# Optimization experiments

Hardware: AMD Instinct MI355X
Metric: run time of the kernel (lower is better)

## Reference

```python
import jax, jax.numpy as jnp
import numpy as np

B, T, F, G, H, N, C = 32, 64, 32, 32, 256, 20000, 32
EPS = 1e-5


def setup_inputs() -> dict:
    key = jax.random.key(0)
    ks = jax.random.split(key, 24)
    s = 0.05
    d = {}
    d["data_feats"] = jax.random.normal(ks[0], (B, T, F), jnp.float32)
    d["gat_output"] = jax.random.normal(ks[1], (B, N, G), jnp.float32)
    d["row_ids"] = jax.random.randint(ks[2], (B, T), 0, 2 * N, jnp.int32)
    d["node_ids"] = jax.random.randint(ks[3], (N,), 0, 2 * N, jnp.int32)
    # shared LSTM (2 layers): layer0 input F+G, layer1 input H; b = b_ih + b_hh fused
    d["shared_Wih0"] = jax.random.normal(ks[4], (4 * H, F + G)) * s
    d["shared_Whh0"] = jax.random.normal(ks[5], (4 * H, H)) * s
    d["shared_b0"] = jax.random.normal(ks[6], (4 * H,)) * s
    d["shared_Wih1"] = jax.random.normal(ks[7], (4 * H, H)) * s
    d["shared_Whh1"] = jax.random.normal(ks[8], (4 * H, H)) * s
    d["shared_b1"] = jax.random.normal(ks[9], (4 * H,)) * s
    # act/time/timeR LSTMs stacked on leading axis 3, each 2 layers of [4H,H]
    d["heads_Wih"] = jax.random.normal(ks[10], (3, 2, 4 * H, H)) * s
    d["heads_Whh"] = jax.random.normal(ks[11], (3, 2, 4 * H, H)) * s
    d["heads_b"] = jax.random.normal(ks[12], (3, 2, 4 * H)) * s
    d["bn_gnn_g"] = jnp.ones((G,), jnp.float32)
    d["bn_gnn_b"] = jnp.zeros((G,), jnp.float32)
    d["bn_shared_g"] = jnp.ones((H,), jnp.float32)
    d["bn_shared_b"] = jnp.zeros((H,), jnp.float32)
    d["heads_bn_g"] = jnp.ones((3, H), jnp.float32)
    d["heads_bn_b"] = jnp.zeros((3, H), jnp.float32)
    d["fc_act_W"] = jax.random.normal(ks[13], (C, H)) * s
    d["fc_act_b"] = jnp.zeros((C,), jnp.float32)
    d["fc_time_W"] = jax.random.normal(ks[14], (1, H)) * s
    d["fc_time_b"] = jnp.zeros((1,), jnp.float32)
    d["fc_timeR_W"] = jax.random.normal(ks[15], (1, H)) * s
    d["fc_timeR_b"] = jnp.zeros((1,), jnp.float32)
    return d


def batchnorm(x, gamma, beta):
    # BatchNorm1d training-mode: stats over (batch, length) per channel; x: [B, L, C]
    mean = jnp.mean(x, axis=(0, 1))
    var = jnp.var(x, axis=(0, 1))
    return (x - mean) * (gamma / jnp.sqrt(var + EPS)) + beta


def lstm_layer(x, Wih, Whh, b):
    # x: [B, T, Din]; PyTorch gate order i, f, g, o
    xp = jnp.einsum("btf,gf->btg", x, Wih) + b  # [B, T, 4H]
    h = Whh.shape[1]
    init = (jnp.zeros((x.shape[0], h), x.dtype), jnp.zeros((x.shape[0], h), x.dtype))

    def step(carry, xt):
        hprev, cprev = carry
        gates = xt + hprev @ Whh.T
        i, f, g, o = jnp.split(gates, 4, axis=-1)
        c = jax.nn.sigmoid(f) * cprev + jax.nn.sigmoid(i) * jnp.tanh(g)
        hnew = jax.nn.sigmoid(o) * jnp.tanh(c)
        return (hnew, c), hnew

    _, hs = jax.lax.scan(step, init, jnp.swapaxes(xp, 0, 1))
    return jnp.swapaxes(hs, 0, 1)  # [B, T, H]


def reference(data_feats, gat_output, row_ids, node_ids,
              shared_Wih0, shared_Whh0, shared_b0,
              shared_Wih1, shared_Whh1, shared_b1,
              heads_Wih, heads_Whh, heads_b,
              bn_gnn_g, bn_gnn_b, bn_shared_g, bn_shared_b,
              heads_bn_g, heads_bn_b,
              fc_act_W, fc_act_b, fc_time_W, fc_time_b, fc_timeR_W, fc_timeR_b):
    # --- graph branch: BN over GAT output, value-match lookup + gather ---
    gat_norm = batchnorm(gat_output, bn_gnn_g, bn_gnn_b)  # [B, N, G]
    eq = row_ids[:, :, None] == node_ids[None, None, :]   # [B, T, N]
    idx = jnp.argmax(eq, axis=-1)                          # first matching index
    found = jnp.any(eq, axis=-1)
    gathered = jnp.take_along_axis(gat_norm, idx[:, :, None], axis=1)  # [B, T, G]
    matched = jnp.where(found[:, :, None], gathered, 0.0)
    lstm_in = jnp.concatenate([data_feats, matched], axis=-1)  # [B, T, F+G]

    # --- shared 2-layer LSTM + BN (dropout off / eval) ---
    shared = lstm_layer(lstm_in, shared_Wih0, shared_Whh0, shared_b0)
    shared = lstm_layer(shared, shared_Wih1, shared_Whh1, shared_b1)
    shared = batchnorm(shared, bn_shared_g, bn_shared_b)

    # --- act / time / timeR head LSTMs (vmapped over the 3 heads) + BN ---
    def head(Wih, Whh, b, g, bb):
        hh = lstm_layer(shared, Wih[0], Whh[0], b[0])
        hh = lstm_layer(hh, Wih[1], Whh[1], b[1])
        return batchnorm(hh, g, bb)

    heads = jax.vmap(head)(heads_Wih, heads_Whh, heads_b, heads_bn_g, heads_bn_b)
    last = heads[:, :, -1, :]  # [3, B, H]

    act = jax.nn.softmax(last[0] @ fc_act_W.T + fc_act_b, axis=1)
    time = last[1] @ fc_time_W.T + fc_time_b
    timeR = last[2] @ fc_timeR_W.T + fc_timeR_b
    return act, time, timeR
```

## Files before the change

### kernel.cpp

```cpp
#include <hip/hip_runtime.h>
#include <hip/hip_fp16.h>
#include <math.h>

#define Bn 32
#define Tn 64
#define Fdim 32
#define Gdim 32
#define Hdim 256
#define Ndim 20000
#define Cdim 32
#define G4 1024
#define BT 2048
#define EPSc 1e-5f

__device__ __forceinline__ float sigmoidf_(float x){ return 1.0f/(1.0f + __expf(-x)); }
__device__ __forceinline__ float tanhf_(float x){ return 2.0f/(1.0f+__expf(-2.0f*x)) - 1.0f; }

typedef _Float16 h2t __attribute__((ext_vector_type(2)));

__device__ __forceinline__ float fdot2_(unsigned w, unsigned h, float acc){
#if defined(__has_builtin) && __has_builtin(__builtin_amdgcn_fdot2)
  return __builtin_amdgcn_fdot2(__builtin_bit_cast(h2t, w), __builtin_bit_cast(h2t, h), acc, false);
#else
  h2t a = __builtin_bit_cast(h2t, w), b = __builtin_bit_cast(h2t, h);
  acc = fmaf((float)a.x, (float)b.x, acc);
  return fmaf((float)a.y, (float)b.y, acc);
#endif
}

__device__ __forceinline__ unsigned packh_(float lo, float hi){
  unsigned ulo = (unsigned)__half_as_ushort(__float2half(lo));
  unsigned uhi = (unsigned)__half_as_ushort(__float2half(hi));
  return ulo | (uhi << 16);
}

__global__ void init_kernel(float* ws){
  int i = blockIdx.x*256 + threadIdx.x;
  if (i < 2112) ws[i] = 0.0f;
  int* table = (int*)(ws + 2112);
  if (i < 40000) table[i] = 0x7fffffff;
}

__global__ void bn_stats_kernel(const float* __restrict__ gat, float* __restrict__ sums){
  __shared__ float ss[256], sq[256];
  int tid = threadIdx.x;
  int idx = blockIdx.x*256 + tid;
  int stride = gridDim.x*256;
  const int total = Bn*Ndim*Gdim;
  float s=0.f,q=0.f;
  for (int i=idx; i<total; i+=stride){ float v = gat[i]; s+=v; q+=v*v; }
  ss[tid]=s; sq[tid]=q; __syncthreads();
  for (int off=128; off>=32; off>>=1){
    if(tid<off){ ss[tid]+=ss[tid+off]; sq[tid]+=sq[tid+off]; }
    __syncthreads();
  }
  if (tid<32){ atomicAdd(&sums[tid], ss[tid]); atomicAdd(&sums[32+tid], sq[tid]); }
}

__global__ void table_kernel(const int* __restrict__ node_ids, int* __restrict__ table){
  int i = blockIdx.x*256 + threadIdx.x;
  if (i < Ndim) atomicMin(&table[node_ids[i]], i);
}

__global__ void build_input_kernel(const float* __restrict__ feats, const float* __restrict__ gat,
    const int* __restrict__ row_ids, const int* __restrict__ table, const float* __restrict__ sums,
    const float* __restrict__ bng, const float* __restrict__ bnb, unsigned* __restrict__ out){
  int gt = blockIdx.x*256 + threadIdx.x;
  int pos = gt >> 5; int k2 = gt & 31;
  float lo, hi;
  if (k2 < 16){
    float2 v = *(const float2*)(feats + pos*Fdim + 2*k2);
    lo = v.x; hi = v.y;
  } else {
    int g0 = 2*(k2-16);
    int r = row_ids[pos];
    int idx = table[r];
    if (idx < Ndim){
      int b = pos / Tn;
      float2 x = *(const float2*)(gat + (size_t)(b*Ndim + idx)*Gdim + g0);
      const float cnt = (float)(Bn*Ndim);
      float m0 = sums[g0]/cnt,   v0 = sums[32+g0]/cnt - m0*m0;
      float m1 = sums[g0+1]/cnt, v1 = sums[32+g0+1]/cnt - m1*m1;
      lo = (x.x-m0)*bng[g0]*rsqrtf(v0+EPSc) + bnb[g0];
      hi = (x.y-m1)*bng[g0+1]*rsqrtf(v1+EPSc) + bnb[g0+1];
    } else { lo = 0.0f; hi = 0.0f; }
  }
  out[gt] = packh_(lo, hi);
}

struct TArgs { const float* src[8]; unsigned* dst[8]; int K[8]; };
__global__ void packwih_kernel(TArgs a){
  __shared__ unsigned tile[32][33];
  int mat = blockIdx.y;
  int K = a.K[mat];
  int K2 = K >> 1;
  int ktiles = K2 >> 5;
  int tk = blockIdx.x & 3;
  int tn = blockIdx.x >> 2;
  if (tk >= ktiles) return;
  const float* src = a.src[mat];
  unsigned* dst = a.dst[mat];
  int tx = threadIdx.x, ty = threadIdx.y;
  int n0 = tn*32, k2_0 = tk*32;
  #pragma unroll
  for (int i=0;i<4;i++){
    int nn = ty + 8*i;
    const float* p = src + (size_t)(n0+nn)*K + 2*(k2_0 + tx);
    tile[nn][tx] = packh_(p[0], p[1]);
  }
  __syncthreads();
  #pragma unroll
  for (int i=0;i<4;i++){
    int r = ty + 8*i;
    dst[(size_t)(k2_0 + r)*G4 + n0 + tx] = tile[tx][r];
  }
}

struct PkArgs { const float* src[8]; };
__global__ void pack_kernel(PkArgs a, unsigned* __restrict__ dst){
  int gid = blockIdx.x*256 + threadIdx.x;
  int m = gid >> 17;
  int rem = gid & 0x1FFFF;
  int q = rem & 3;
  int t2 = (rem >> 2) & 1023;
  int ci = rem >> 12;
  int c = ci >> 3, i = ci & 7;
  int j = t2 & 255, kq = t2 >> 8;
  int r = 4*j + c;
  int k = kq*64 + 8*i + 2*q;
  const float* W = a.src[m];
  dst[gid] = packh_(W[r*256 + k], W[r*256 + k + 1]);
}

struct PArgs { const unsigned* x[3]; const unsigned* wt[3]; const float* bias[3]; float* out[3]; int K2; };
__global__ __launch_bounds__(256) void proj_kernel(PArgs a){
  int hd = blockIdx.z;
  int n  = blockIdx.y*256 + threadIdx.x;
  int m0 = blockIdx.x*8;
  int K2 = a.K2;
  const unsigned* xh = a.x[hd] + (size_t)m0*K2;
  const unsigned* wt = a.wt[hd];
  float bv = a.bias[hd][n];
  float acc[8];
  #pragma unroll
  for (int i=0;i<8;i++) acc[i]=bv;
  for (int k2=0;k2<K2;k2+=4){
    unsigned w0 = wt[(size_t)(k2+0)*G4+n];
    unsigned w1 = wt[(size_t)(k2+1)*G4+n];
    unsigned w2 = wt[(size_t)(k2+2)*G4+n];
    unsigned w3 = wt[(size_t)(k2+3)*G4+n];
    #pragma unroll
    for (int i=0;i<8;i++){
      uint4 xv = *(const uint4*)(xh + i*K2 + k2);
      acc[i]=fdot2_(w0,xv.x,acc[i]); acc[i]=fdot2_(w1,xv.y,acc[i]);
      acc[i]=fdot2_(w2,xv.z,acc[i]); acc[i]=fdot2_(w3,xv.w,acc[i]);
    }
  }
  float* out = a.out[hd] + (size_t)m0*G4 + n;
  #pragma unroll
  for (int i=0;i<8;i++) out[i*G4]=acc[i];
}

struct RArgs { const float* xp[3]; const unsigned* wt[3]; float* out[3]; unsigned* outh[3]; int f32out; int f16out; };
__global__ __launch_bounds__(1024,1) void rec_kernel(RArgs a){
  extern __shared__ float lds[];
  unsigned* lw   = (unsigned*)lds;
  float*    part = lds + 32768;
  unsigned* hp   = (unsigned*)(lds + 36864);
  int b = blockIdx.x, hd = blockIdx.y, tid = threadIdx.x;
  int j = tid & 255, kq = tid >> 8;
  const float* xp = a.xp[hd] + (size_t)b*Tn*G4;
  const unsigned* wt = a.wt[hd];
  float* out = a.out[hd] + (size_t)b*Tn*Hdim;
  unsigned* outh = a.outh[hd] + (size_t)b*Tn*128;
  int f32o = a.f32out, f16o = a.f16out;

  unsigned w[96];
  #pragma unroll
  for (int c=0;c<4;c++){
    #pragma unroll
    for (int i=0;i<6;i++){
      uint4 v = *(const uint4*)(wt + ((c*8+i)*1024 + tid)*4);
      w[(c*6+i)*4+0]=v.x; w[(c*6+i)*4+1]=v.y; w[(c*6+i)*4+2]=v.z; w[(c*6+i)*4+3]=v.w;
    }
    #pragma unroll
    for (int i=6;i<8;i++){
      uint4 v = *(const uint4*)(wt + ((c*8+i)*1024 + tid)*4);
      *(uint4*)(lw + ((c*2+(i-6))*1024 + tid)*4) = v;
    }
  }
  float cst = 0.0f;
  if (tid < 128){ hp[tid] = 0u; hp[128+tid] = 0u; }
  float4 xc = make_float4(0.f,0.f,0.f,0.f);
  if (kq == 0) xc = *(const float4*)(xp + 4*j);
  __syncthreads();

  int p = 0;
  for (int t=0; t<Tn; t++){
    float4 xn = xc;
    if (kq == 0) xn = *(const float4*)(xp + (size_t)(t+1)*G4 + 4*j);
    float ac0, ac1, ac2, ac3;
    if (kq == 0){ ac0=xc.x; ac1=xc.y; ac2=xc.z; ac3=xc.w; }
    else        { ac0=0.f; ac1=0.f; ac2=0.f; ac3=0.f; }
    const unsigned* hrow = hp + p*128 + kq*32;
    #pragma unroll
    for (int ic=0; ic<6; ic++){
      uint4 hv = *(const uint4*)(hrow + 4*ic);
      ac0=fdot2_(w[0*24+ic*4+0],hv.x,ac0); ac0=fdot2_(w[0*24+ic*4+1],hv.y,ac0);
      ac0=fdot2_(w[0*24+ic*4+2],hv.z,ac0); ac0=fdot2_(w[0*24+ic*4+3],hv.w,ac0);
      ac1=fdot2_(w[1*24+ic*4+0],hv.x,ac1); ac1=fdot2_(w[1*24+ic*4+1],hv.y,ac1);
      ac1=fdot2_(w[1*24+ic*4+2],hv.z,ac1); ac1=fdot2_(w[1*24+ic*4+3],hv.w,ac1);
      ac2=fdot2_(w[2*24+ic*4+0],hv.x,ac2); ac2=fdot2_(w[2*24+ic*4+1],hv.y,ac2);
      ac2=fdot2_(w[2*24+ic*4+2],hv.z,ac2); ac2=fdot2_(w[2*24+ic*4+3],hv.w,ac2);
      ac3=fdot2_(w[3*24+ic*4+0],hv.x,ac3); ac3=fdot2_(w[3*24+ic*4+1],hv.y,ac3);
      ac3=fdot2_(w[3*24+ic*4+2],hv.z,ac3); ac3=fdot2_(w[3*24+ic*4+3],hv.w,ac3);
    }
    #pragma unroll
    for (int ic=6; ic<8; ic++){
      uint4 hv = *(const uint4*)(hrow + 4*ic);
      { uint4 lv = *(const uint4*)(lw + ((0*2+(ic-6))*1024 + tid)*4);
        ac0=fdot2_(lv.x,hv.x,ac0); ac0=fdot2_(lv.y,hv.y,ac0);
        ac0=fdot2_(lv.z,hv.z,ac0); ac0=fdot2_(lv.w,hv.w,ac0); }
      { uint4 lv = *(const uint4*)(lw + ((1*2+(ic-6))*1024 + tid)*4);
        ac1=fdot2_(lv.x,hv.x,ac1); ac1=fdot2_(lv.y,hv.y,ac1);
        ac1=fdot2_(lv.z,hv.z,ac1); ac1=fdot2_(lv.w,hv.w,ac1); }
      { uint4 lv = *(const uint4*)(lw + ((2*2+(ic-6))*1024 + tid)*4);
        ac2=fdot2_(lv.x,hv.x,ac2); ac2=fdot2_(lv.y,hv.y,ac2);
        ac2=fdot2_(lv.z,hv.z,ac2); ac2=fdot2_(lv.w,hv.w,ac2); }
      { uint4 lv = *(const uint4*)(lw + ((3*2+(ic-6))*1024 + tid)*4);
        ac3=fdot2_(lv.x,hv.x,ac3); ac3=fdot2_(lv.y,hv.y,ac3);
        ac3=fdot2_(lv.z,hv.z,ac3); ac3=fdot2_(lv.w,hv.w,ac3); }
    }
    *(float4*)(part + kq*1024 + 4*j) = make_float4(ac0,ac1,ac2,ac3);
    asm volatile("s_waitcnt lgkmcnt(0)" ::: "memory");
    __builtin_amdgcn_s_barrier();
    if (tid < 256){
      int u = tid;
      float gi = part[u]     + part[1024+u]     + part[2048+u]     + part[3072+u];
      float gf = part[256+u] + part[1024+256+u] + part[2048+256+u] + part[3072+256+u];
      float gg = part[512+u] + part[1024+512+u] + part[2048+512+u] + part[3072+512+u];
      float go = part[768+u] + part[1024+768+u] + part[2048+768+u] + part[3072+768+u];
      cst = sigmoidf_(gf)*cst + sigmoidf_(gi)*tanhf_(gg);
      float h = sigmoidf_(go)*tanhf_(cst);
      if (f32o) out[t*Hdim + u] = h;
      float hpartner = __shfl_xor(h, 1);
      if ((u & 1) == 0){
        unsigned hh = packh_(h, hpartner);
        hp[(p^1)*128 + (u>>1)] = hh;
        if (f16o) outh[t*128 + (u>>1)] = hh;
      }
    }
    asm volatile("s_waitcnt lgkmcnt(0)" ::: "memory");
    __builtin_amdgcn_s_barrier();
    p ^= 1;
    xc = xn;
  }
}

struct SArgs { const float* in[3]; float* stats[3]; };
__global__ void stats_kernel(SArgs a){
  int hd = blockIdx.y; int tid = threadIdx.x;
  const float* in = a.in[hd] + blockIdx.x*256*Hdim;
  float s=0.f,q=0.f;
  for (int r=0;r<256;r++){ float v = in[r*Hdim + tid]; s+=v; q+=v*v; }
  atomicAdd(&a.stats[hd][tid], s);
  atomicAdd(&a.stats[hd][Hdim+tid], q);
}

__global__ void norm_kernel(const float* __restrict__ in, const float* __restrict__ stats,
   const float* __restrict__ g, const float* __restrict__ bta, unsigned* __restrict__ outh){
  int i2 = blockIdx.x*256 + threadIdx.x;
  int h2 = i2 & 127; int m = i2 >> 7;
  int h0 = 2*h2;
  float2 v = *(const float2*)(in + (size_t)m*Hdim + h0);
  float m0 = stats[h0]*(1.0f/BT),   v0 = stats[Hdim+h0]*(1.0f/BT) - m0*m0;
  float m1 = stats[h0+1]*(1.0f/BT), v1 = stats[Hdim+h0+1]*(1.0f/BT) - m1*m1;
  float lo = (v.x-m0)*g[h0]*rsqrtf(v0+EPSc) + bta[h0];
  float hi = (v.y-m1)*g[h0+1]*rsqrtf(v1+EPSc) + bta[h0+1];
  outh[i2] = packh_(lo, hi);
}

__global__ __launch_bounds__(256) void final_kernel(
  const float* __restrict__ h0, const float* __restrict__ h1, const float* __restrict__ h2,
  const float* __restrict__ stats,
  const float* __restrict__ hbg, const float* __restrict__ hbb,
  const float* __restrict__ actW, const float* __restrict__ actB,
  const float* __restrict__ tW, const float* __restrict__ tB,
  const float* __restrict__ rW, const float* __restrict__ rB,
  float* __restrict__ outp){
  __shared__ float v0[Bn*Hdim];
  __shared__ float lg[Bn*Cdim];
  int tid = threadIdx.x;
  for (int i=tid; i<Bn*Hdim; i+=256){
    int b=i>>8, h=i&255;
    float sm = stats[512 + h], sq = stats[512+256+h];
    float mean = sm*(1.0f/BT); float var = sq*(1.0f/BT) - mean*mean;
    v0[i] = (h0[(b*Tn+63)*Hdim + h] - mean)*hbg[h]*rsqrtf(var+EPSc) + hbb[h];
  }
  __syncthreads();
  for (int i=tid; i<Bn*Cdim; i+=256){
    int b=i>>5, cc=i&31;
    float acc = actB[cc];
    const float* wrow = actW + cc*Hdim;
    const float* vrow = v0 + b*Hdim;
    #pragma unroll 4
    for (int h=0;h<Hdim;h++) acc = fmaf(vrow[h], wrow[h], acc);
    lg[i] = acc;
  }
  __syncthreads();
  if (tid < Bn){
    int b = tid;
    float m = -1e30f;
    #pragma unroll
    for (int cc=0; cc<Cdim; cc++) m = fmaxf(m, lg[b*Cdim+cc]);
    float e[Cdim]; float s = 0.f;
    #pragma unroll
    for (int cc=0; cc<Cdim; cc++){ float ee = __expf(lg[b*Cdim+cc]-m); e[cc]=ee; s+=ee; }
    float inv = 1.0f/s;
    #pragma unroll
    for (int cc=0; cc<Cdim; cc++) outp[b*Cdim+cc] = e[cc]*inv;
  }
  if (tid < 64){
    int b = tid & 31; int w = tid >> 5;
    const float* hh = w ? h2 : h1;
    const float* fw = w ? rW : tW;
    float fb = w ? rB[0] : tB[0];
    int hd = 1 + w;
    float acc = fb;
    for (int h=0; h<Hdim; h++){
      float sm = stats[(1+hd)*512 + h], sq = stats[(1+hd)*512+256+h];
      float mean = sm*(1.0f/BT); float var = sq*(1.0f/BT) - mean*mean;
      float v = (hh[(b*Tn+63)*Hdim + h] - mean)*hbg[hd*Hdim+h]*rsqrtf(var+EPSc) + hbb[hd*Hdim+h];
      acc = fmaf(v, fw[h], acc);
    }
    outp[1024 + w*32 + b] = acc;
  }
}

extern "C" void kernel_launch(void* const* d_in, const int* in_sizes, int n_in,
                              void* d_out, int out_size, void* d_ws, size_t ws_size,
                              hipStream_t stream){
  const float* data_feats = (const float*)d_in[0];
  const float* gat   = (const float*)d_in[1];
  const int*   row_ids  = (const int*)d_in[2];
  const int*   node_ids = (const int*)d_in[3];
  const float* sWih0 = (const float*)d_in[4];
  const float* sWhh0 = (const float*)d_in[5];
  const float* sb0   = (const float*)d_in[6];
  const float* sWih1 = (const float*)d_in[7];
  const float* sWhh1 = (const float*)d_in[8];
  const float* sb1   = (const float*)d_in[9];
  const float* hWih  = (const float*)d_in[10];
  const float* hWhh  = (const float*)d_in[11];
  const float* hb    = (const float*)d_in[12];
  const float* bng   = (const float*)d_in[13];
  const float* bnb   = (const float*)d_in[14];
  const float* bsg   = (const float*)d_in[15];
  const float* bsb   = (const float*)d_in[16];
  const float* hbg   = (const float*)d_in[17];
  const float* hbb   = (const float*)d_in[18];
  const float* actW  = (const float*)d_in[19];
  const float* actB  = (const float*)d_in[20];
  const float* tW    = (const float*)d_in[21];
  const float* tB    = (const float*)d_in[22];
  const float* rW    = (const float*)d_in[23];
  const float* rB    = (const float*)d_in[24];
  float* ws  = (float*)d_ws;
  float* out = (float*)d_out;

  const size_t S_GAT = 0;
  const size_t S_BN  = 64;
  const size_t TABLE = 2112;
  const size_t WIHP  = 42112;
  const size_t PSLOT = 131072;
  const size_t WHHP  = WIHP + 8*PSLOT;
  const size_t LSTM_INH = WHHP + 8*PSLOT;
  const size_t XPOFF = LSTM_INH + 65536;
  const size_t BUF0H = XPOFF + 3*2097152;
  const size_t BUF1  = BUF0H + 262144;
  const size_t BUFNH = BUF1 + 524288;
  const size_t HB0H  = BUFNH + 262144;
  const size_t HB1   = HB0H + 3*262144;

  const int REC_LDS = 148480;
  hipFuncSetAttribute((const void*)rec_kernel, hipFuncAttributeMaxDynamicSharedMemorySize, REC_LDS);

  init_kernel<<<157,256,0,stream>>>(ws);
  bn_stats_kernel<<<2048,256,0,stream>>>(gat, ws+S_GAT);
  table_kernel<<<(Ndim+255)/256,256,0,stream>>>(node_ids, (int*)(ws+TABLE));
  build_input_kernel<<<256,256,0,stream>>>(data_feats, gat, row_ids, (int*)(ws+TABLE),
                                           ws+S_GAT, bng, bnb, (unsigned*)(ws+LSTM_INH));

  unsigned* wih = (unsigned*)(ws + WIHP);
  TArgs ta;
  ta.src[0]=sWih0; ta.K[0]=64;
  ta.src[1]=sWih1; ta.K[1]=256;
  for (int hd=0; hd<3; hd++) for (int l=0;l<2;l++){
    ta.src[2+hd*2+l] = hWih + (size_t)(hd*2+l)*G4*Hdim; ta.K[2+hd*2+l] = 256;
  }
  for (int i=0;i<8;i++) ta.dst[i] = wih + (size_t)i*PSLOT;
  packwih_kernel<<<dim3(128,8),dim3(32,8),0,stream>>>(ta);

  unsigned* whh = (unsigned*)(ws + WHHP);
  PkArgs pka;
  pka.src[0]=sWhh0; pka.src[1]=sWhh1;
  for (int hd=0; hd<3; hd++) for (int l=0;l<2;l++)
    pka.src[2+hd*2+l] = hWhh + (size_t)(hd*2+l)*G4*Hdim;
  pack_kernel<<<4096,256,0,stream>>>(pka, whh);

  PArgs pa; RArgs ra; SArgs sa;
  pa.K2=32; pa.x[0]=(unsigned*)(ws+LSTM_INH); pa.wt[0]=wih+0*PSLOT; pa.bias[0]=sb0; pa.out[0]=ws+XPOFF;
  proj_kernel<<<dim3(256,4,1),256,0,stream>>>(pa);
  ra.xp[0]=ws+XPOFF; ra.wt[0]=whh+0*PSLOT; ra.out[0]=ws+BUF1; ra.outh[0]=(unsigned*)(ws+BUF0H);
  ra.f32out=0; ra.f16out=1;
  rec_kernel<<<dim3(32,1),1024,REC_LDS,stream>>>(ra);
  pa.K2=128; pa.x[0]=(unsigned*)(ws+BUF0H); pa.wt[0]=wih+1*PSLOT; pa.bias[0]=sb1; pa.out[0]=ws+XPOFF;
  proj_kernel<<<dim3(256,4,1),256,0,stream>>>(pa);
  ra.xp[0]=ws+XPOFF; ra.wt[0]=whh+1*PSLOT; ra.out[0]=ws+BUF1; ra.outh[0]=(unsigned*)(ws+BUF0H);
  ra.f32out=1; ra.f16out=0;
  rec_kernel<<<dim3(32,1),1024,REC_LDS,stream>>>(ra);
  sa.in[0]=ws+BUF1; sa.stats[0]=ws+S_BN;
  stats_kernel<<<dim3(8,1),256,0,stream>>>(sa);
  norm_kernel<<<1024,256,0,stream>>>(ws+BUF1, ws+S_BN, bsg, bsb, (unsigned*)(ws+BUFNH));
  pa.K2=128;
  for (int hd=0;hd<3;hd++){
    pa.x[hd]=(unsigned*)(ws+BUFNH); pa.wt[hd]=wih+(size_t)(2+hd*2)*PSLOT; pa.bias[hd]=hb + (size_t)(hd*2)*G4;
    pa.out[hd]=ws+XPOFF+(size_t)hd*2097152;
  }
  proj_kernel<<<dim3(256,4,3),256,0,stream>>>(pa);
  for (int hd=0;hd<3;hd++){
    ra.xp[hd]=ws+XPOFF+(size_t)hd*2097152; ra.wt[hd]=whh+(size_t)(2+hd*2)*PSLOT;
    ra.out[hd]=ws+HB1+(size_t)hd*524288; ra.outh[hd]=(unsigned*)(ws+HB0H)+(size_t)hd*262144;
  }
  ra.f32out=0; ra.f16out=1;
  rec_kernel<<<dim3(32,3),1024,REC_LDS,stream>>>(ra);
  for (int hd=0;hd<3;hd++){
    pa.x[hd]=(unsigned*)(ws+HB0H)+(size_t)hd*262144; pa.wt[hd]=wih+(size_t)(2+hd*2+1)*PSLOT;
    pa.bias[hd]=hb + (size_t)(hd*2+1)*G4;
    pa.out[hd]=ws+XPOFF+(size_t)hd*2097152;
  }
  proj_kernel<<<dim3(256,4,3),256,0,stream>>>(pa);
  for (int hd=0;hd<3;hd++){
    ra.xp[hd]=ws+XPOFF+(size_t)hd*2097152; ra.wt[hd]=whh+(size_t)(2+hd*2+1)*PSLOT;
    ra.out[hd]=ws+HB1+(size_t)hd*524288; ra.outh[hd]=(unsigned*)(ws+HB0H)+(size_t)hd*262144;
  }
  ra.f32out=1; ra.f16out=0;
  rec_kernel<<<dim3(32,3),1024,REC_LDS,stream>>>(ra);
  for (int hd=0;hd<3;hd++){ sa.in[hd]=ws+HB1+(size_t)hd*524288; sa.stats[hd]=ws+S_BN+(size_t)(1+hd)*512; }
  stats_kernel<<<dim3(8,3),256,0,stream>>>(sa);
  final_kernel<<<1,256,0,stream>>>(ws+HB1, ws+HB1+524288, ws+HB1+2*524288, ws+S_BN,
                                   hbg, hbb, actW, actB, tW, tB, rW, rB, out);
}
```

Baseline: 898.7 us.

## Give each recurrent thread a full gate row and combine gates via DPP

The recurrent LSTM kernel is remapped so each of the 1024 threads computes one full gate row over all 256 hidden inputs, with the four gates of a unit sitting in adjacent lanes. The gate values are exchanged with DPP broadcasts instead of going through an LDS partial-sum buffer. This removes one barrier and the LDS reduction per timestep, and every thread now applies the nonlinearity. The weight packing kernel is rewritten to match the new layout. The cost is that every thread reads the whole hidden vector from LDS each step, and the next-step input prefetch is dropped.

```diff
diff --git a/kernel.cpp b/kernel.cpp
--- a/kernel.cpp
+++ b/kernel.cpp
@@ -32,6 +32,15 @@
   unsigned ulo = (unsigned)__half_as_ushort(__float2half(lo));
   unsigned uhi = (unsigned)__half_as_ushort(__float2half(hi));
   return ulo | (uhi << 16);
+}
+
+__device__ __forceinline__ float dppbc_(float y, int ctrl){
+  switch (ctrl){
+    case 0:  return __builtin_bit_cast(float, __builtin_amdgcn_mov_dpp(__builtin_bit_cast(int,y), 0x00, 0xF, 0xF, true));
+    case 1:  return __builtin_bit_cast(float, __builtin_amdgcn_mov_dpp(__builtin_bit_cast(int,y), 0x55, 0xF, 0xF, true));
+    case 2:  return __builtin_bit_cast(float, __builtin_amdgcn_mov_dpp(__builtin_bit_cast(int,y), 0xAA, 0xF, 0xF, true));
+    default: return __builtin_bit_cast(float, __builtin_amdgcn_mov_dpp(__builtin_bit_cast(int,y), 0xFF, 0xF, 0xF, true));
+  }
 }
 
 __global__ void init_kernel(float* ws){
@@ -120,16 +129,15 @@
 __global__ void pack_kernel(PkArgs a, unsigned* __restrict__ dst){
   int gid = blockIdx.x*256 + threadIdx.x;
   int m = gid >> 17;
-  int rem = gid & 0x1FFFF;
-  int q = rem & 3;
-  int t2 = (rem >> 2) & 1023;
-  int ci = rem >> 12;
-  int c = ci >> 3, i = ci & 7;
-  int j = t2 & 255, kq = t2 >> 8;
-  int r = 4*j + c;
-  int k = kq*64 + 8*i + 2*q;
+  int idx = gid & 0x1FFFF;
+  int e  = idx >> 12;
+  int t1 = (idx >> 2) & 1023;
+  int d4 = idx & 3;
+  int u = t1 >> 2, g = t1 & 3;
+  int rr = g*256 + u;
+  int k = 8*e + 2*d4;
   const float* W = a.src[m];
-  dst[gid] = packh_(W[r*256 + k], W[r*256 + k + 1]);
+  dst[gid] = packh_(W[rr*256 + k], W[rr*256 + k + 1]);
 }
 
 struct PArgs { const unsigned* x[3]; const unsigned* wt[3]; const float* bias[3]; float* out[3]; int K2; };
@@ -164,11 +172,11 @@
 struct RArgs { const float* xp[3]; const unsigned* wt[3]; float* out[3]; unsigned* outh[3]; int f32out; int f16out; };
 __global__ __launch_bounds__(1024,1) void rec_kernel(RArgs a){
   extern __shared__ float lds[];
-  unsigned* lw   = (unsigned*)lds;
-  float*    part = lds + 32768;
-  unsigned* hp   = (unsigned*)(lds + 36864);
+  unsigned* lw = (unsigned*)lds;
+  unsigned* hp = (unsigned*)lds + 32768;
   int b = blockIdx.x, hd = blockIdx.y, tid = threadIdx.x;
-  int j = tid & 255, kq = tid >> 8;
+  int u = tid >> 2, gsel = tid & 3;
+  int r = gsel*256 + u;
   const float* xp = a.xp[hd] + (size_t)b*Tn*G4;
   const unsigned* wt = a.wt[hd];
   float* out = a.out[hd] + (size_t)b*Tn*Hdim;
@@ -177,83 +185,63 @@
 
   unsigned w[96];
   #pragma unroll
-  for (int c=0;c<4;c++){
-    #pragma unroll
-    for (int i=0;i<6;i++){
-      uint4 v = *(const uint4*)(wt + ((c*8+i)*1024 + tid)*4);
-      w[(c*6+i)*4+0]=v.x; w[(c*6+i)*4+1]=v.y; w[(c*6+i)*4+2]=v.z; w[(c*6+i)*4+3]=v.w;
-    }
-    #pragma unroll
-    for (int i=6;i<8;i++){
-      uint4 v = *(const uint4*)(wt + ((c*8+i)*1024 + tid)*4);
-      *(uint4*)(lw + ((c*2+(i-6))*1024 + tid)*4) = v;
-    }
-  }
+  for (int e=0;e<24;e++){
+    uint4 v = *(const uint4*)(wt + (size_t)(e*1024 + tid)*4);
+    w[4*e+0]=v.x; w[4*e+1]=v.y; w[4*e+2]=v.z; w[4*e+3]=v.w;
+  }
+  #pragma unroll
+  for (int e=24;e<32;e++){
+    uint4 v = *(const uint4*)(wt + (size_t)(e*1024 + tid)*4);
+    *(uint4*)(lw + ((e-24)*1024 + tid)*4) = v;
+  }
+  if (tid < 256) hp[tid] = 0u;
   float cst = 0.0f;
-  if (tid < 128){ hp[tid] = 0u; hp[128+tid] = 0u; }
-  float4 xc = make_float4(0.f,0.f,0.f,0.f);
-  if (kq == 0) xc = *(const float4*)(xp + 4*j);
+  const float ab  = (gsel==2) ? 2.0f : 1.0f;
+  const float cof = (gsel==2) ? -1.0f : 0.0f;
   __syncthreads();
 
   int p = 0;
   for (int t=0; t<Tn; t++){
-    float4 xn = xc;
-    if (kq == 0) xn = *(const float4*)(xp + (size_t)(t+1)*G4 + 4*j);
-    float ac0, ac1, ac2, ac3;
-    if (kq == 0){ ac0=xc.x; ac1=xc.y; ac2=xc.z; ac3=xc.w; }
-    else        { ac0=0.f; ac1=0.f; ac2=0.f; ac3=0.f; }
-    const unsigned* hrow = hp + p*128 + kq*32;
-    #pragma unroll
-    for (int ic=0; ic<6; ic++){
-      uint4 hv = *(const uint4*)(hrow + 4*ic);
-      ac0=fdot2_(w[0*24+ic*4+0],hv.x,ac0); ac0=fdot2_(w[0*24+ic*4+1],hv.y,ac0);
-      ac0=fdot2_(w[0*24+ic*4+2],hv.z,ac0); ac0=fdot2_(w[0*24+ic*4+3],hv.w,ac0);
-      ac1=fdot2_(w[1*24+ic*4+0],hv.x,ac1); ac1=fdot2_(w[1*24+ic*4+1],hv.y,ac1);
-      ac1=fdot2_(w[1*24+ic*4+2],hv.z,ac1); ac1=fdot2_(w[1*24+ic*4+3],hv.w,ac1);
-      ac2=fdot2_(w[2*24+ic*4+0],hv.x,ac2); ac2=fdot2_(w[2*24+ic*4+1],hv.y,ac2);
-      ac2=fdot2_(w[2*24+ic*4+2],hv.z,ac2); ac2=fdot2_(w[2*24+ic*4+3],hv.w,ac2);
-      ac3=fdot2_(w[3*24+ic*4+0],hv.x,ac3); ac3=fdot2_(w[3*24+ic*4+1],hv.y,ac3);
-      ac3=fdot2_(w[3*24+ic*4+2],hv.z,ac3); ac3=fdot2_(w[3*24+ic*4+3],hv.w,ac3);
+    float xv = xp[(size_t)t*G4 + r];
+    const unsigned* hb = hp + p*128;
+    float acc0=0.f, acc1=0.f;
+    #pragma unroll
+    for (int j=0;j<24;j+=2){
+      uint4 h0 = *(const uint4*)(hb + 4*j);
+      uint4 h1 = *(const uint4*)(hb + 4*j + 4);
+      acc0=fdot2_(w[4*j+0],h0.x,acc0); acc1=fdot2_(w[4*j+4],h1.x,acc1);
+      acc0=fdot2_(w[4*j+1],h0.y,acc0); acc1=fdot2_(w[4*j+5],h1.y,acc1);
+      acc0=fdot2_(w[4*j+2],h0.z,acc0); acc1=fdot2_(w[4*j+6],h1.z,acc1);
+      acc0=fdot2_(w[4*j+3],h0.w,acc0); acc1=fdot2_(w[4*j+7],h1.w,acc1);
     }
     #pragma unroll
-    for (int ic=6; ic<8; ic++){
-      uint4 hv = *(const uint4*)(hrow + 4*ic);
-      { uint4 lv = *(const uint4*)(lw + ((0*2+(ic-6))*1024 + tid)*4);
-        ac0=fdot2_(lv.x,hv.x,ac0); ac0=fdot2_(lv.y,hv.y,ac0);
-        ac0=fdot2_(lv.z,hv.z,ac0); ac0=fdot2_(lv.w,hv.w,ac0); }
-      { uint4 lv = *(const uint4*)(lw + ((1*2+(ic-6))*1024 + tid)*4);
-        ac1=fdot2_(lv.x,hv.x,ac1); ac1=fdot2_(lv.y,hv.y,ac1);
-        ac1=fdot2_(lv.z,hv.z,ac1); ac1=fdot2_(lv.w,hv.w,ac1); }
-      { uint4 lv = *(const uint4*)(lw + ((2*2+(ic-6))*1024 + tid)*4);
-        ac2=fdot2_(lv.x,hv.x,ac2); ac2=fdot2_(lv.y,hv.y,ac2);
-        ac2=fdot2_(lv.z,hv.z,ac2); ac2=fdot2_(lv.w,hv.w,ac2); }
-      { uint4 lv = *(const uint4*)(lw + ((3*2+(ic-6))*1024 + tid)*4);
-        ac3=fdot2_(lv.x,hv.x,ac3); ac3=fdot2_(lv.y,hv.y,ac3);
-        ac3=fdot2_(lv.z,hv.z,ac3); ac3=fdot2_(lv.w,hv.w,ac3); }
+    for (int j=24;j<32;j+=2){
+      uint4 h0 = *(const uint4*)(hb + 4*j);
+      uint4 h1 = *(const uint4*)(hb + 4*j + 4);
+      uint4 l0 = *(const uint4*)(lw + ((j-24)*1024 + tid)*4);
+      uint4 l1 = *(const uint4*)(lw + ((j-23)*1024 + tid)*4);
+      acc0=fdot2_(l0.x,h0.x,acc0); acc1=fdot2_(l1.x,h1.x,acc1);
+      acc0=fdot2_(l0.y,h0.y,acc0); acc1=fdot2_(l1.y,h1.y,acc1);
+      acc0=fdot2_(l0.z,h0.z,acc0); acc1=fdot2_(l1.z,h1.z,acc1);
+      acc0=fdot2_(l0.w,h0.w,acc0); acc1=fdot2_(l1.w,h1.w,acc1);
     }
-    *(float4*)(part + kq*1024 + 4*j) = make_float4(ac0,ac1,ac2,ac3);
-    asm volatile("s_waitcnt lgkmcnt(0)" ::: "memory");
-    __builtin_amdgcn_s_barrier();
-    if (tid < 256){
-      int u = tid;
-      float gi = part[u]     + part[1024+u]     + part[2048+u]     + part[3072+u];
-      float gf = part[256+u] + part[1024+256+u] + part[2048+256+u] + part[3072+256+u];
-      float gg = part[512+u] + part[1024+512+u] + part[2048+512+u] + part[3072+512+u];
-      float go = part[768+u] + part[1024+768+u] + part[2048+768+u] + part[3072+768+u];
-      cst = sigmoidf_(gf)*cst + sigmoidf_(gi)*tanhf_(gg);
-      float h = sigmoidf_(go)*tanhf_(cst);
-      if (f32o) out[t*Hdim + u] = h;
-      float hpartner = __shfl_xor(h, 1);
-      if ((u & 1) == 0){
-        unsigned hh = packh_(h, hpartner);
-        hp[(p^1)*128 + (u>>1)] = hh;
-        if (f16o) outh[t*128 + (u>>1)] = hh;
-      }
+    float acc = acc0 + acc1 + xv;
+    float ex = __expf(-ab*acc);
+    float y  = ab/(1.0f+ex) + cof;
+    float vi = dppbc_(y,0), vf = dppbc_(y,1), vg = dppbc_(y,2), vo = dppbc_(y,3);
+    cst = fmaf(vf, cst, vi*vg);
+    float h = vo * tanhf_(cst);
+    if (f32o && gsel==0) out[t*Hdim + u] = h;
+    float hpart = __shfl_xor(h, 4);
+    if ((tid & 7) == 0){
+      unsigned hh = packh_(h, hpart);
+      int m = tid >> 3;
+      hp[(p^1)*128 + m] = hh;
+      if (f16o) outh[t*128 + m] = hh;
     }
     asm volatile("s_waitcnt lgkmcnt(0)" ::: "memory");
     __builtin_amdgcn_s_barrier();
     p ^= 1;
-    xc = xn;
   }
 }
 
@@ -382,7 +370,7 @@
   const size_t HB0H  = BUFNH + 262144;
   const size_t HB1   = HB0H + 3*262144;
 
-  const int REC_LDS = 148480;
+  const int REC_LDS = 132096;
   hipFuncSetAttribute((const void*)rec_kernel, hipFuncAttributeMaxDynamicSharedMemorySize, REC_LDS);
 
   init_kernel<<<157,256,0,stream>>>(ws);
```

New measurement: 916.9 us. 2.0% more time.
